# Kernel tuning notes

Hardware: AMD Instinct MI355X
Metric: run time of the kernel (lower is better)

## Reference

```python
import jax, jax.numpy as jnp
import numpy as np

HEADS = 16


def setup_inputs() -> dict:
    key = jax.random.key(0)
    ks = jax.random.split(key, 6)
    b, n, c = 4, 2048, 1024  # batch, seq_len, query_dim (== hidden_dim)
    h = 1024                 # hidden_dim = heads * dim_head = 16 * 64
    s = 0.02
    return {
        "x": jax.random.normal(ks[0], (b, n, c), jnp.float32),
        "Wq": jax.random.normal(ks[1], (h, c), jnp.float32) * s,
        "Wk": jax.random.normal(ks[2], (h, c), jnp.float32) * s,
        "Wv": jax.random.normal(ks[3], (h, c), jnp.float32) * s,
        "Wout": jax.random.normal(ks[4], (c, h), jnp.float32) * s,
        "bout": jnp.zeros((c,), jnp.float32),
    }


def reference(x, Wq, Wk, Wv, Wout, bout):
    # x: (b, n, c). Self-attention (context = x).
    b, n, c = x.shape
    m = HEADS
    d = Wq.shape[0] // m  # dim_head
    # 1x1 conv == linear projection over channel dim
    q = jnp.einsum('bnc,hc->bnh', x, Wq).reshape(b, n, m, d)
    k = jnp.einsum('bnc,hc->bnh', x, Wk).reshape(b, n, m, d)
    v = jnp.einsum('bnc,hc->bnh', x, Wv).reshape(b, n, m, d)
    scale = d ** (-0.25)  # 1/sqrt(sqrt(d)), applied to both q and k
    # weight: (b, m, n_q, n_k)
    weight = jnp.einsum('bimd,bjmd->bmij', q * scale, k * scale)
    weight = jax.nn.softmax(weight, axis=-1)
    a = jnp.einsum('bmij,bjmd->bimd', weight, v).reshape(b, n, m * d)
    return jnp.einsum('bnh,ch->bnc', a, Wout) + bout
```

## Files before the change

### kernel.cpp

```cpp
#include <hip/hip_runtime.h>
#include <stdint.h>
#include <stddef.h>

typedef __attribute__((ext_vector_type(4))) float f32x4;
typedef __attribute__((ext_vector_type(16))) float f32x16;
typedef __attribute__((ext_vector_type(8))) short s16x8;
typedef __attribute__((ext_vector_type(4))) short s16x4;

__device__ __forceinline__ short f2bf(float f) {
  uint32_t u = __builtin_bit_cast(uint32_t, f);
  uint32_t r = (u + 0x7fffu + ((u >> 16) & 1u)) >> 16;
  return (short)r;
}

__device__ __forceinline__ void gload_lds16(const void* g, void* l) {
  __builtin_amdgcn_global_load_lds(
      (const __attribute__((address_space(1))) void*)g,
      (__attribute__((address_space(3))) void*)l, 16, 0, 0);
}

__device__ __forceinline__ int msk8(int r) { return (r & 7) ^ ((r >> 3) & 7); }
__device__ __forceinline__ int swz(int r, int c) {
  return r * 64 + (c ^ (msk8(r) << 3));
}
__device__ __forceinline__ int swv(int d) { return d ^ ((d >> 3) & 3); }

__global__ __launch_bounds__(256) void cvt_kernel(const float* __restrict__ src,
                                                  short* __restrict__ dst, int n4) {
  int i = blockIdx.x * blockDim.x + threadIdx.x;
  if (i >= n4) return;
  float4 v = reinterpret_cast<const float4*>(src)[i];
  s16x4 o;
  o[0] = f2bf(v.x); o[1] = f2bf(v.y); o[2] = f2bf(v.z); o[3] = f2bf(v.w);
  reinterpret_cast<s16x4*>(dst)[i] = o;
}

__global__ __launch_bounds__(256) void cvt_w(const float* __restrict__ Wq,
                                             const float* __restrict__ Wk,
                                             const float* __restrict__ Wv,
                                             const float* __restrict__ Wout,
                                             short* __restrict__ Wqkv,
                                             short* __restrict__ Woutb) {
  int i = blockIdx.x * 256 + threadIdx.x;
  int g = i >> 18, li = i & 262143;
  const float* src = g == 0 ? Wq : g == 1 ? Wk : g == 2 ? Wv : Wout;
  short* dst = g < 3 ? Wqkv + (size_t)g * 1048576 : Woutb;
  float4 v = reinterpret_cast<const float4*>(src)[li];
  s16x4 o;
  o[0] = f2bf(v.x); o[1] = f2bf(v.y); o[2] = f2bf(v.z); o[3] = f2bf(v.w);
  reinterpret_cast<s16x4*>(dst)[li] = o;
}

__global__ __launch_bounds__(256) void gemm_bt(const short* __restrict__ A,
                                               const short* __restrict__ B,
                                               short* __restrict__ Cb,
                                               int M, int N, int K,
                                               float qscl, int qcols) {
  __shared__ short lA[128 * 64];
  __shared__ short lB[128 * 64];
  const int tid = threadIdx.x;
  const int lane = tid & 63, wid = tid >> 6;
  const int g = lane >> 4, li = lane & 15;
  const int nbx = N >> 7;
  const int q8 = gridDim.x >> 3;
  const int orig = blockIdx.x;
  const int bswz = (orig & 7) * q8 + (orig >> 3);
  const int by = bswz / nbx, bx = bswz % nbx;
  const int brow = by << 7, bcol = bx << 7;
  const int wr = (wid >> 1) << 6, wc = (wid & 1) << 6;

  f32x4 acc[4][4] = {};

  for (int k0 = 0; k0 < K; k0 += 64) {
    __syncthreads();
#pragma unroll
    for (int i = 0; i < 4; i++) {
      int j = tid + i * 256;
      int r = j >> 3, s = j & 7;
      gload_lds16(A + (size_t)(brow + r) * K + k0 + 8 * (s ^ msk8(r)), &lA[j * 8]);
    }
#pragma unroll
    for (int i = 0; i < 4; i++) {
      int j = tid + i * 256;
      int r = j >> 3, s = j & 7;
      gload_lds16(B + (size_t)(bcol + r) * K + k0 + 8 * (s ^ msk8(r)), &lB[j * 8]);
    }
    __syncthreads();
#pragma unroll
    for (int ks = 0; ks < 2; ks++) {
      s16x8 af[4], bfr[4];
#pragma unroll
      for (int ai = 0; ai < 4; ai++) {
        int row = wr + ai * 16 + li;
        af[ai] = *(const s16x8*)&lA[swz(row, ks * 32 + g * 8)];
      }
#pragma unroll
      for (int bj = 0; bj < 4; bj++) {
        int row = wc + bj * 16 + li;
        bfr[bj] = *(const s16x8*)&lB[swz(row, ks * 32 + g * 8)];
      }
#pragma unroll
      for (int ai = 0; ai < 4; ai++)
#pragma unroll
        for (int bj = 0; bj < 4; bj++)
          acc[ai][bj] = __builtin_amdgcn_mfma_f32_16x16x32_bf16(af[ai], bfr[bj],
                                                               acc[ai][bj], 0, 0, 0);
    }
  }

#pragma unroll
  for (int ai = 0; ai < 4; ai++) {
#pragma unroll
    for (int bj = 0; bj < 4; bj++) {
#pragma unroll
      for (int e = 0; e < 4; e++) {
        int row = brow + wr + ai * 16 + g * 4 + e;
        int col = bcol + wc + bj * 16 + li;
        float v = acc[ai][bj][e];
        if (col < qcols) v *= qscl;
        Cb[(size_t)row * N + col] = f2bf(v);
      }
    }
  }
}

__global__ __launch_bounds__(256) void gemm_bt64(const short* __restrict__ A,
                                                 const short* __restrict__ B,
                                                 float* __restrict__ C,
                                                 const float* __restrict__ bias,
                                                 int M, int N, int K) {
  __shared__ short lA[64 * 64];
  __shared__ short lB[128 * 64];
  const int tid = threadIdx.x;
  const int lane = tid & 63, wid = tid >> 6;
  const int g = lane >> 4, li = lane & 15;
  const int nbx = N >> 7;
  const int q8 = gridDim.x >> 3;
  const int orig = blockIdx.x;
  const int bswz = (orig & 7) * q8 + (orig >> 3);
  const int by = bswz / nbx, bx = bswz % nbx;
  const int brow = by << 6, bcol = bx << 7;
  const int wr = (wid >> 1) << 5, wc = (wid & 1) << 6;

  f32x4 acc[2][4] = {};

  for (int k0 = 0; k0 < K; k0 += 64) {
    __syncthreads();
#pragma unroll
    for (int i = 0; i < 2; i++) {
      int j = tid + i * 256;
      int r = j >> 3, s = j & 7;
      gload_lds16(A + (size_t)(brow + r) * K + k0 + 8 * (s ^ msk8(r)), &lA[j * 8]);
    }
#pragma unroll
    for (int i = 0; i < 4; i++) {
      int j = tid + i * 256;
      int r = j >> 3, s = j & 7;
      gload_lds16(B + (size_t)(bcol + r) * K + k0 + 8 * (s ^ msk8(r)), &lB[j * 8]);
    }
    __syncthreads();
#pragma unroll
    for (int ks = 0; ks < 2; ks++) {
      s16x8 af[2], bfr[4];
#pragma unroll
      for (int ai = 0; ai < 2; ai++) {
        int row = wr + ai * 16 + li;
        af[ai] = *(const s16x8*)&lA[swz(row, ks * 32 + g * 8)];
      }
#pragma unroll
      for (int bj = 0; bj < 4; bj++) {
        int row = wc + bj * 16 + li;
        bfr[bj] = *(const s16x8*)&lB[swz(row, ks * 32 + g * 8)];
      }
#pragma unroll
      for (int ai = 0; ai < 2; ai++)
#pragma unroll
        for (int bj = 0; bj < 4; bj++)
          acc[ai][bj] = __builtin_amdgcn_mfma_f32_16x16x32_bf16(af[ai], bfr[bj],
                                                               acc[ai][bj], 0, 0, 0);
    }
  }

#pragma unroll
  for (int ai = 0; ai < 2; ai++) {
#pragma unroll
    for (int bj = 0; bj < 4; bj++) {
#pragma unroll
      for (int e = 0; e < 4; e++) {
        int row = brow + wr + ai * 16 + g * 4 + e;
        int col = bcol + wc + bj * 16 + li;
        C[(size_t)row * N + col] = acc[ai][bj][e] + bias[col];
      }
    }
  }
}

__global__ __launch_bounds__(256, 4) void attn_kernel(const short* __restrict__ qkv,
                                                      short* __restrict__ aout) {
  __shared__ short lds[2][8192];

  const int tid = threadIdx.x;
  const int lane = tid & 63, w = tid >> 6;
  const int l31 = lane & 31, hi = lane >> 5;
  const int bid = blockIdx.x;
  const int qt = bid & 15, head = (bid >> 4) & 15, b = bid >> 8;
  const int row0 = b * 2048;
  const int qrow = qt * 128 + w * 32 + l31;
  const int qcol = head * 64, kcol = 1024 + head * 64, vcol = 2048 + head * 64;

#pragma unroll
  for (int s = 0; s < 4; s++)
    gload_lds16(qkv + (size_t)(row0 + qrow) * 3072 + qcol + 16 * s + 8 * hi,
                &lds[0][(w * 4 + s) * 512]);
  __syncthreads();
  s16x8 qf[4];
#pragma unroll
  for (int s = 0; s < 4; s++)
    qf[s] = *(const s16x8*)&lds[0][(w * 4 + s) * 512 + lane * 8];
  __syncthreads();

  const int vj = tid >> 3, va = tid & 7;
  const int vks = vj >> 4;
  const int vphi = (vj >> 2) & 1;
  const int veV = (vj & 3) + 4 * ((vj >> 3) & 1);
  const int vdd = va >> 2, va3 = va & 3;
  const int vbase = (vks * 2 + vdd) * 512 + vphi * 256 + va3 * 64 + veV;
  const int vslot_r = (32 * hi + swv(l31)) * 8;

#pragma unroll
  for (int sub = 0; sub < 2; sub++)
    gload_lds16(qkv + (size_t)(row0 + sub * 32 + l31) * 3072 + kcol + 16 * w + 8 * hi,
                &lds[0][(sub * 4 + w) * 512]);
#pragma unroll
  for (int sub = 0; sub < 2; sub++) {
    s16x8 v0 = *(const s16x8*)(qkv + (size_t)(row0 + sub * 32 + vj) * 3072 + vcol + 8 * va);
#pragma unroll
    for (int t2 = 0; t2 < 8; t2++)
      lds[0][4096 + sub * 2048 + vbase + 8 * (t2 ^ va3)] = v0[t2];
  }
  __syncthreads();

  f32x16 acc0 = {}, acc1 = {};
  float l_r = 0.f;

  for (int jt = 0; jt < 32; jt++) {
    const int cur = jt & 1, nxt = cur ^ 1;
    const int jnext = (jt + 1) * 64;
    const bool pf = (jt < 31);

    s16x8 vs0, vs1;
    if (pf) {
      vs0 = *(const s16x8*)(qkv + (size_t)(row0 + jnext + vj) * 3072 + vcol + 8 * va);
      vs1 = *(const s16x8*)(qkv + (size_t)(row0 + jnext + 32 + vj) * 3072 + vcol + 8 * va);
#pragma unroll
      for (int sub = 0; sub < 2; sub++)
        gload_lds16(qkv + (size_t)(row0 + jnext + sub * 32 + l31) * 3072 + kcol +
                        16 * w + 8 * hi,
                    &lds[nxt][(sub * 4 + w) * 512]);
    }

    f32x16 st0 = {}, st1 = {};
    const short* lc = &lds[cur][0];
    __builtin_amdgcn_s_setprio(1);
#pragma unroll
    for (int s = 0; s < 4; s++) {
      s16x8 kf0 = *(const s16x8*)&lc[s * 512 + lane * 8];
      s16x8 kf1 = *(const s16x8*)&lc[(4 + s) * 512 + lane * 8];
      st0 = __builtin_amdgcn_mfma_f32_32x32x16_bf16(kf0, qf[s], st0, 0, 0, 0);
      st1 = __builtin_amdgcn_mfma_f32_32x32x16_bf16(kf1, qf[s], st1, 0, 0, 0);
    }
    __builtin_amdgcn_s_setprio(0);

#pragma unroll
    for (int r = 0; r < 16; r++) st0[r] = exp2f(st0[r]);
#pragma unroll
    for (int r = 0; r < 16; r++) st1[r] = exp2f(st1[r]);
    f32x16 sm = st0 + st1;
#pragma unroll
    for (int r = 0; r < 8; r++) sm[r] = sm[r] + sm[r + 8];
#pragma unroll
    for (int r = 0; r < 4; r++) sm[r] = sm[r] + sm[r + 4];
    float rs = (sm[0] + sm[1]) + (sm[2] + sm[3]);
    rs += __shfl_xor(rs, 32, 64);
    l_r += rs;

    if (pf) {
      short* dst = &lds[nxt][4096];
#pragma unroll
      for (int t2 = 0; t2 < 8; t2++) {
        int off = vbase + 8 * (t2 ^ va3);
        dst[off] = vs0[t2];
        dst[2048 + off] = vs1[t2];
      }
    }

    const short* lV = &lds[cur][4096];
    __builtin_amdgcn_s_setprio(1);
#pragma unroll
    for (int sub = 0; sub < 2; sub++) {
      const f32x16& pp = sub ? st1 : st0;
#pragma unroll
      for (int ks = 0; ks < 2; ks++) {
        int w0, w1, w2, w3;
        asm("v_cvt_pk_bf16_f32 %0, %1, %2" : "=v"(w0) : "v"(pp[8*ks+0]), "v"(pp[8*ks+1]));
        asm("v_cvt_pk_bf16_f32 %0, %1, %2" : "=v"(w1) : "v"(pp[8*ks+2]), "v"(pp[8*ks+3]));
        asm("v_cvt_pk_bf16_f32 %0, %1, %2" : "=v"(w2) : "v"(pp[8*ks+4]), "v"(pp[8*ks+5]));
        asm("v_cvt_pk_bf16_f32 %0, %1, %2" : "=v"(w3) : "v"(pp[8*ks+6]), "v"(pp[8*ks+7]));
        int4 paw;
        paw.x = w0; paw.y = w1; paw.z = w2; paw.w = w3;
        s16x8 pa = __builtin_bit_cast(s16x8, paw);
        s16x8 v0 = *(const s16x8*)&lV[sub * 2048 + (ks * 2 + 0) * 512 + vslot_r];
        s16x8 v1 = *(const s16x8*)&lV[sub * 2048 + (ks * 2 + 1) * 512 + vslot_r];
        acc0 = __builtin_amdgcn_mfma_f32_32x32x16_bf16(v0, pa, acc0, 0, 0, 0);
        acc1 = __builtin_amdgcn_mfma_f32_32x32x16_bf16(v1, pa, acc1, 0, 0, 0);
      }
    }
    __builtin_amdgcn_s_setprio(0);

    __syncthreads();
  }

  float inv = 1.f / l_r;
  const size_t rowoff = (size_t)(row0 + qt * 128 + w * 32 + l31) * 1024 + head * 64;
#pragma unroll
  for (int rq = 0; rq < 4; rq++) {
    s16x4 o0, o1;
#pragma unroll
    for (int i2 = 0; i2 < 4; i2++) {
      o0[i2] = f2bf(acc0[rq * 4 + i2] * inv);
      o1[i2] = f2bf(acc1[rq * 4 + i2] * inv);
    }
    int dbase = 8 * rq + 4 * hi;
    *(s16x4*)&aout[rowoff + dbase] = o0;
    *(s16x4*)&aout[rowoff + 32 + dbase] = o1;
  }
}

extern "C" void kernel_launch(void* const* d_in, const int* in_sizes, int n_in,
                              void* d_out, int out_size, void* d_ws, size_t ws_size,
                              hipStream_t stream) {
  const float* x    = (const float*)d_in[0];
  const float* Wq   = (const float*)d_in[1];
  const float* Wk   = (const float*)d_in[2];
  const float* Wv   = (const float*)d_in[3];
  const float* Wout = (const float*)d_in[4];
  const float* bout = (const float*)d_in[5];
  float* out = (float*)d_out;

  char* ws = (char*)d_ws;
  short* xb    = (short*)(ws);
  short* Wqkv  = (short*)(ws + (16ull << 20));
  short* Woutb = (short*)(ws + (22ull << 20));
  short* qkv   = (short*)(ws + (24ull << 20));
  short* a_ws  = xb;

  const float SCL = 0.125f * 1.44269504088896f;

  cvt_kernel<<<8192, 256, 0, stream>>>(x, xb, 2097152);
  cvt_w<<<4096, 256, 0, stream>>>(Wq, Wk, Wv, Wout, Wqkv, Woutb);

  gemm_bt<<<64 * 24, 256, 0, stream>>>(xb, Wqkv, qkv, 8192, 3072, 1024, SCL, 1024);

  attn_kernel<<<1024, 256, 0, stream>>>(qkv, a_ws);

  gemm_bt64<<<1024, 256, 0, stream>>>(a_ws, Woutb, out, bout, 8192, 1024, 1024);
}
```

Before: 283.0 us.

## Pre-transpose V into MFMA-ready tiles and compute row sums via MFMA

A new kernel writes V once per (batch, head, key tile) in the swizzled LDS layout the attention kernel expects. The attention loop can then load V with direct global-to-LDS copies instead of per-element scalar LDS stores, and the two-stage loop is unrolled so buffer pointers are static. The softmax denominator is now computed by an extra MFMA against a vector of ones, replacing the VALU reduction and cross-lane shuffle. The cost is an extra launch, an extra V write and read through global memory, and one more MFMA per sub-step.

```diff
diff --git a/kernel.cpp b/kernel.cpp
--- a/kernel.cpp
+++ b/kernel.cpp
@@ -195,7 +195,37 @@
   }
 }
 
+__global__ __launch_bounds__(256) void vt_kernel(const short* __restrict__ qkv,
+                                                 short* __restrict__ vt) {
+  __shared__ short tile[4096];
+  const int tid = threadIdx.x;
+  const int bid = blockIdx.x;
+  const int kt = bid & 31, head = (bid >> 5) & 15, b = bid >> 9;
+  const int row0 = b * 2048 + kt * 64;
+  const int vcol = 2048 + head * 64;
+  const int vj = tid >> 3, va = tid & 7;
+  const int vks = vj >> 4;
+  const int vphi = (vj >> 2) & 1;
+  const int veV = (vj & 3) + 4 * ((vj >> 3) & 1);
+  const int vdd = va >> 2, va3 = va & 3;
+  const int vbase = (vks * 2 + vdd) * 512 + vphi * 256 + va3 * 64 + veV;
+
+#pragma unroll
+  for (int sub = 0; sub < 2; sub++) {
+    s16x8 v = *(const s16x8*)(qkv + (size_t)(row0 + sub * 32 + vj) * 3072 + vcol + 8 * va);
+#pragma unroll
+    for (int t2 = 0; t2 < 8; t2++)
+      tile[sub * 2048 + vbase + 8 * (t2 ^ va3)] = v[t2];
+  }
+  __syncthreads();
+  short* dst = vt + (size_t)bid * 4096;
+#pragma unroll
+  for (int i = 0; i < 2; i++)
+    *(s16x8*)&dst[i * 2048 + tid * 8] = *(const s16x8*)&tile[i * 2048 + tid * 8];
+}
+
 __global__ __launch_bounds__(256, 4) void attn_kernel(const short* __restrict__ qkv,
+                                                      const short* __restrict__ vt,
                                                       short* __restrict__ aout) {
   __shared__ short lds[2][8192];
 
@@ -206,7 +236,8 @@
   const int qt = bid & 15, head = (bid >> 4) & 15, b = bid >> 8;
   const int row0 = b * 2048;
   const int qrow = qt * 128 + w * 32 + l31;
-  const int qcol = head * 64, kcol = 1024 + head * 64, vcol = 2048 + head * 64;
+  const int qcol = head * 64, kcol = 1024 + head * 64;
+  const short* vtb = vt + ((size_t)(b * 512 + head * 32)) * 4096;
 
 #pragma unroll
   for (int s = 0; s < 4; s++)
@@ -219,12 +250,6 @@
     qf[s] = *(const s16x8*)&lds[0][(w * 4 + s) * 512 + lane * 8];
   __syncthreads();
 
-  const int vj = tid >> 3, va = tid & 7;
-  const int vks = vj >> 4;
-  const int vphi = (vj >> 2) & 1;
-  const int veV = (vj & 3) + 4 * ((vj >> 3) & 1);
-  const int vdd = va >> 2, va3 = va & 3;
-  const int vbase = (vks * 2 + vdd) * 512 + vphi * 256 + va3 * 64 + veV;
   const int vslot_r = (32 * hi + swv(l31)) * 8;
 
 #pragma unroll
@@ -232,95 +257,81 @@
     gload_lds16(qkv + (size_t)(row0 + sub * 32 + l31) * 3072 + kcol + 16 * w + 8 * hi,
                 &lds[0][(sub * 4 + w) * 512]);
 #pragma unroll
-  for (int sub = 0; sub < 2; sub++) {
-    s16x8 v0 = *(const s16x8*)(qkv + (size_t)(row0 + sub * 32 + vj) * 3072 + vcol + 8 * va);
-#pragma unroll
-    for (int t2 = 0; t2 < 8; t2++)
-      lds[0][4096 + sub * 2048 + vbase + 8 * (t2 ^ va3)] = v0[t2];
-  }
+  for (int i = 0; i < 2; i++)
+    gload_lds16(vtb + (w * 2 + i) * 512 + lane * 8, &lds[0][4096 + (w * 2 + i) * 512]);
   __syncthreads();
 
-  f32x16 acc0 = {}, acc1 = {};
-  float l_r = 0.f;
-
-  for (int jt = 0; jt < 32; jt++) {
-    const int cur = jt & 1, nxt = cur ^ 1;
-    const int jnext = (jt + 1) * 64;
-    const bool pf = (jt < 31);
-
-    s16x8 vs0, vs1;
-    if (pf) {
-      vs0 = *(const s16x8*)(qkv + (size_t)(row0 + jnext + vj) * 3072 + vcol + 8 * va);
-      vs1 = *(const s16x8*)(qkv + (size_t)(row0 + jnext + 32 + vj) * 3072 + vcol + 8 * va);
-#pragma unroll
-      for (int sub = 0; sub < 2; sub++)
-        gload_lds16(qkv + (size_t)(row0 + jnext + sub * 32 + l31) * 3072 + kcol +
-                        16 * w + 8 * hi,
-                    &lds[nxt][(sub * 4 + w) * 512]);
-    }
-
-    f32x16 st0 = {}, st1 = {};
-    const short* lc = &lds[cur][0];
-    __builtin_amdgcn_s_setprio(1);
-#pragma unroll
-    for (int s = 0; s < 4; s++) {
-      s16x8 kf0 = *(const s16x8*)&lc[s * 512 + lane * 8];
-      s16x8 kf1 = *(const s16x8*)&lc[(4 + s) * 512 + lane * 8];
-      st0 = __builtin_amdgcn_mfma_f32_32x32x16_bf16(kf0, qf[s], st0, 0, 0, 0);
-      st1 = __builtin_amdgcn_mfma_f32_32x32x16_bf16(kf1, qf[s], st1, 0, 0, 0);
-    }
-    __builtin_amdgcn_s_setprio(0);
-
-#pragma unroll
-    for (int r = 0; r < 16; r++) st0[r] = exp2f(st0[r]);
-#pragma unroll
-    for (int r = 0; r < 16; r++) st1[r] = exp2f(st1[r]);
-    f32x16 sm = st0 + st1;
-#pragma unroll
-    for (int r = 0; r < 8; r++) sm[r] = sm[r] + sm[r + 8];
-#pragma unroll
-    for (int r = 0; r < 4; r++) sm[r] = sm[r] + sm[r + 4];
-    float rs = (sm[0] + sm[1]) + (sm[2] + sm[3]);
-    rs += __shfl_xor(rs, 32, 64);
-    l_r += rs;
-
-    if (pf) {
-      short* dst = &lds[nxt][4096];
-#pragma unroll
-      for (int t2 = 0; t2 < 8; t2++) {
-        int off = vbase + 8 * (t2 ^ va3);
-        dst[off] = vs0[t2];
-        dst[2048 + off] = vs1[t2];
-      }
-    }
-
-    const short* lV = &lds[cur][4096];
-    __builtin_amdgcn_s_setprio(1);
-#pragma unroll
-    for (int sub = 0; sub < 2; sub++) {
-      const f32x16& pp = sub ? st1 : st0;
-#pragma unroll
-      for (int ks = 0; ks < 2; ks++) {
-        int w0, w1, w2, w3;
-        asm("v_cvt_pk_bf16_f32 %0, %1, %2" : "=v"(w0) : "v"(pp[8*ks+0]), "v"(pp[8*ks+1]));
-        asm("v_cvt_pk_bf16_f32 %0, %1, %2" : "=v"(w1) : "v"(pp[8*ks+2]), "v"(pp[8*ks+3]));
-        asm("v_cvt_pk_bf16_f32 %0, %1, %2" : "=v"(w2) : "v"(pp[8*ks+4]), "v"(pp[8*ks+5]));
-        asm("v_cvt_pk_bf16_f32 %0, %1, %2" : "=v"(w3) : "v"(pp[8*ks+6]), "v"(pp[8*ks+7]));
-        int4 paw;
-        paw.x = w0; paw.y = w1; paw.z = w2; paw.w = w3;
-        s16x8 pa = __builtin_bit_cast(s16x8, paw);
-        s16x8 v0 = *(const s16x8*)&lV[sub * 2048 + (ks * 2 + 0) * 512 + vslot_r];
-        s16x8 v1 = *(const s16x8*)&lV[sub * 2048 + (ks * 2 + 1) * 512 + vslot_r];
-        acc0 = __builtin_amdgcn_mfma_f32_32x32x16_bf16(v0, pa, acc0, 0, 0, 0);
-        acc1 = __builtin_amdgcn_mfma_f32_32x32x16_bf16(v1, pa, acc1, 0, 0, 0);
-      }
-    }
-    __builtin_amdgcn_s_setprio(0);
-
-    __syncthreads();
-  }
-
-  float inv = 1.f / l_r;
+  f32x16 acc0 = {}, acc1 = {}, asum = {};
+  s16x8 ones;
+#pragma unroll
+  for (int i = 0; i < 8; i++) ones[i] = (short)0x3F80;
+
+  for (int jt2 = 0; jt2 < 16; jt2++) {
+#pragma unroll
+    for (int half = 0; half < 2; half++) {
+      const int jt = jt2 * 2 + half;
+      short* bufc = (short*)lds[half];
+      short* bufn = (short*)lds[half ^ 1];
+
+      if (jt < 31) {
+        const int jnext = (jt + 1) * 64;
+#pragma unroll
+        for (int sub = 0; sub < 2; sub++)
+          gload_lds16(qkv + (size_t)(row0 + jnext + sub * 32 + l31) * 3072 + kcol +
+                          16 * w + 8 * hi,
+                      &bufn[(sub * 4 + w) * 512]);
+        const short* vsrc = vtb + (size_t)(jt + 1) * 4096;
+#pragma unroll
+        for (int i = 0; i < 2; i++)
+          gload_lds16(vsrc + (w * 2 + i) * 512 + lane * 8,
+                      &bufn[4096 + (w * 2 + i) * 512]);
+      }
+
+      f32x16 st0 = {}, st1 = {};
+      __builtin_amdgcn_s_setprio(1);
+#pragma unroll
+      for (int s = 0; s < 4; s++) {
+        s16x8 kf0 = *(const s16x8*)&bufc[s * 512 + lane * 8];
+        s16x8 kf1 = *(const s16x8*)&bufc[(4 + s) * 512 + lane * 8];
+        st0 = __builtin_amdgcn_mfma_f32_32x32x16_bf16(kf0, qf[s], st0, 0, 0, 0);
+        st1 = __builtin_amdgcn_mfma_f32_32x32x16_bf16(kf1, qf[s], st1, 0, 0, 0);
+      }
+      __builtin_amdgcn_s_setprio(0);
+
+#pragma unroll
+      for (int r = 0; r < 16; r++) st0[r] = exp2f(st0[r]);
+#pragma unroll
+      for (int r = 0; r < 16; r++) st1[r] = exp2f(st1[r]);
+
+      const short* lV = &bufc[4096];
+      __builtin_amdgcn_s_setprio(1);
+#pragma unroll
+      for (int sub = 0; sub < 2; sub++) {
+        const f32x16& pp = sub ? st1 : st0;
+#pragma unroll
+        for (int ks = 0; ks < 2; ks++) {
+          int w0, w1, w2, w3;
+          asm("v_cvt_pk_bf16_f32 %0, %1, %2" : "=v"(w0) : "v"(pp[8*ks+0]), "v"(pp[8*ks+1]));
+          asm("v_cvt_pk_bf16_f32 %0, %1, %2" : "=v"(w1) : "v"(pp[8*ks+2]), "v"(pp[8*ks+3]));
+          asm("v_cvt_pk_bf16_f32 %0, %1, %2" : "=v"(w2) : "v"(pp[8*ks+4]), "v"(pp[8*ks+5]));
+          asm("v_cvt_pk_bf16_f32 %0, %1, %2" : "=v"(w3) : "v"(pp[8*ks+6]), "v"(pp[8*ks+7]));
+          int4 paw;
+          paw.x = w0; paw.y = w1; paw.z = w2; paw.w = w3;
+          s16x8 pa = __builtin_bit_cast(s16x8, paw);
+          s16x8 v0 = *(const s16x8*)&lV[sub * 2048 + (ks * 2 + 0) * 512 + vslot_r];
+          s16x8 v1 = *(const s16x8*)&lV[sub * 2048 + (ks * 2 + 1) * 512 + vslot_r];
+          acc0 = __builtin_amdgcn_mfma_f32_32x32x16_bf16(v0, pa, acc0, 0, 0, 0);
+          acc1 = __builtin_amdgcn_mfma_f32_32x32x16_bf16(v1, pa, acc1, 0, 0, 0);
+          asum = __builtin_amdgcn_mfma_f32_32x32x16_bf16(ones, pa, asum, 0, 0, 0);
+        }
+      }
+      __builtin_amdgcn_s_setprio(0);
+
+      __syncthreads();
+    }
+  }
+
+  float inv = 1.f / asum[0];
   const size_t rowoff = (size_t)(row0 + qt * 128 + w * 32 + l31) * 1024 + head * 64;
 #pragma unroll
   for (int rq = 0; rq < 4; rq++) {
@@ -352,6 +363,7 @@
   short* Wqkv  = (short*)(ws + (16ull << 20));
   short* Woutb = (short*)(ws + (22ull << 20));
   short* qkv   = (short*)(ws + (24ull << 20));
+  short* vt    = (short*)(ws + (72ull << 20));
   short* a_ws  = xb;
 
   const float SCL = 0.125f * 1.44269504088896f;
@@ -361,7 +373,9 @@
 
   gemm_bt<<<64 * 24, 256, 0, stream>>>(xb, Wqkv, qkv, 8192, 3072, 1024, SCL, 1024);
 
-  attn_kernel<<<1024, 256, 0, stream>>>(qkv, a_ws);
+  vt_kernel<<<2048, 256, 0, stream>>>(qkv, vt);
+
+  attn_kernel<<<1024, 256, 0, stream>>>(qkv, vt, a_ws);
 
   gemm_bt64<<<1024, 256, 0, stream>>>(a_ws, Woutb, out, bout, 8192, 1024, 1024);
 }
```

After: 294.3 us. 4.0% more time.
